# Kernel tuning notes

Hardware: AMD Instinct MI355X
Metric: run time of the kernel (lower is better)

## Reference

```python
import jax
jax.config.update("jax_enable_x64", True)
import jax.numpy as jnp
import numpy as np

CKA_WEIGHT = 0.1


def _group_cka_sum(feats):
    """feats: [F, N, D] float. Returns sum of pairwise CKA over all (i,j) pairs.

    Faithful to CKASR: K = X X^T with zeroed diagonal, unbiased HSIC
    (Song et al. estimator), CKA[i,j] = HSIC(Ki,Kj)/sqrt(HSIC(Ki,Ki)HSIC(Kj,Kj)).
    All pairwise loops are batched into einsums.
    """
    F, N, D = feats.shape
    X = feats.reshape(F, N, D).astype(jnp.float64)
    K = jnp.einsum('fnd,fmd->fnm', X, X)                 # [F,N,N] Gram
    K = K * (1.0 - jnp.eye(N, dtype=K.dtype))            # fill_diagonal_(0)
    # HSIC(Ki, Kj) = 1/(N(N-3)) * ( tr(Ki Kj)
    #   + sum(Ki) sum(Kj) / ((N-1)(N-2))
    #   - 2/(N-2) * <rowsum(Ki), rowsum(Kj)> )
    trKL = jnp.einsum('iab,jab->ij', K, K)               # tr(Ki Kj), K symmetric
    s = jnp.sum(K, axis=(1, 2))                          # [F] total sums
    r = jnp.sum(K, axis=2)                               # [F,N] row sums
    rr = jnp.einsum('ia,ja->ij', r, r)                   # [F,F]
    hsic = (trKL + jnp.outer(s, s) / ((N - 1) * (N - 2))
            - 2.0 * rr / (N - 2)) / (N * (N - 3))        # [F,F]
    d = jnp.sqrt(jnp.diagonal(hsic))                     # [F]
    cka = hsic / (d[:, None] * d[None, :])
    return jnp.sum(cka)


def setup_inputs() -> dict:
    key = jax.random.key(0)
    k1, k2, k3, k4 = jax.random.split(key, 4)
    N, C = 64, 1000
    output = jax.random.normal(k1, (N, C), dtype=jnp.float32)
    target = jax.random.randint(k2, (N,), 0, C, dtype=jnp.int64)
    feats_a = jax.random.normal(k3, (3, N, 65536), dtype=jnp.float32)
    feats_b = jax.random.normal(k4, (4, N, 32768), dtype=jnp.float32)
    return {"output": output, "target": target,
            "feats_a": feats_a, "feats_b": feats_b}


def reference(output, target, feats_a, feats_b):
    N = output.shape[0]
    logp = jax.nn.log_softmax(output.astype(jnp.float32), axis=-1)
    ce = -jnp.mean(logp[jnp.arange(N), target])           # CrossEntropyLoss (mean)
    cka = _group_cka_sum(feats_a) + _group_cka_sum(feats_b)
    loss = ce + CKA_WEIGHT * cka.astype(jnp.float32)
    return (loss, output)
```

## Files before the change

kernel.cpp:

```cpp
#include <hip/hip_runtime.h>
#include <math.h>

typedef __attribute__((ext_vector_type(8))) short short8;
typedef __attribute__((ext_vector_type(4))) float f32x4;
typedef __attribute__((ext_vector_type(16))) float f32x16;

#define PSTRIDE 4160

__device__ __forceinline__ unsigned int bf16_rn(float x) {
    unsigned int u = __float_as_uint(x);
    return (u + 0x7FFFu + ((u >> 16) & 1u)) >> 16;
}

__device__ __forceinline__ short8 cvt8(float4 a, float4 b) {
    short8 h;
    h[0] = (short)bf16_rn(a.x); h[1] = (short)bf16_rn(a.y);
    h[2] = (short)bf16_rn(a.z); h[3] = (short)bf16_rn(a.w);
    h[4] = (short)bf16_rn(b.x); h[5] = (short)bf16_rn(b.y);
    h[6] = (short)bf16_rn(b.z); h[7] = (short)bf16_rn(b.w);
    return h;
}

__global__ __launch_bounds__(512, 8) void gram_ce_kernel(
    const float* __restrict__ A, const float* __restrict__ B,
    float* __restrict__ partials, int nfA, int nfB,
    const float* __restrict__ logits, const int* __restrict__ target,
    float* __restrict__ out_copy, float* __restrict__ ce_rows, int ceCount)
{
    __shared__ float smem[4096];
    const int t = threadIdx.x;

    if ((int)blockIdx.x < ceCount) {
        const int row = blockIdx.x;
        const float* x = logits + row * 1000;
        float m = -INFINITY;
        for (int i = t; i < 1000; i += 512) {
            float v = x[i];
            out_copy[row * 1000 + i] = v;
            m = fmaxf(m, v);
        }
        smem[t] = m; __syncthreads();
        for (int s = 256; s > 0; s >>= 1) {
            if (t < s) smem[t] = fmaxf(smem[t], smem[t + s]);
            __syncthreads();
        }
        m = smem[0];
        __syncthreads();
        float ssum = 0.f;
        for (int i = t; i < 1000; i += 512) ssum += expf(x[i] - m);
        smem[t] = ssum; __syncthreads();
        for (int s = 256; s > 0; s >>= 1) {
            if (t < s) smem[t] += smem[t + s];
            __syncthreads();
        }
        if (t == 0) {
            double lse = (double)m + log((double)smem[0]);
            int tg = target[row];
            ce_rows[row] = (float)(-((double)x[tg] - lse));
        }
        return;
    }

    const int gb = blockIdx.x - ceCount;
    const int uA = nfA * 128;
    const float* xf;
    int c, D;
    if (gb < uA) {
        int f = gb >> 7; c = gb & 127; D = 65536;
        xf = A + (size_t)f * 64 * 65536;
    } else {
        int v = gb - uA;
        int f = v >> 6; c = v & 63; D = 32768;
        xf = B + (size_t)f * 64 * 32768;
    }

    const int wave = t >> 6, lane = t & 63;
    const int lr = lane & 31, hi = lane >> 5;

    f32x16 acc = (f32x16)0.f;
    if (wave < 4) {
        const int k0 = c * 512 + wave * 128 + hi * 8;
        const float* pA = xf + (size_t)lr * D + k0;
        const float* pB = xf + (size_t)(32 + lr) * D + k0;
#pragma unroll
        for (int s = 0; s < 8; ++s) {
            float4 a0 = *(const float4*)(pA + s * 16);
            float4 a1 = *(const float4*)(pA + s * 16 + 4);
            float4 b0 = *(const float4*)(pB + s * 16);
            float4 b1 = *(const float4*)(pB + s * 16 + 4);
            short8 fa = cvt8(a0, a1);
            short8 fb = cvt8(b0, b1);
            acc = __builtin_amdgcn_mfma_f32_32x32x16_bf16(fa, fb, acc, 0, 0, 0);
        }
    } else {
        const int rb = (wave >= 6) ? 32 : 0;
        const int k0 = c * 512 + (wave & 1) * 256 + hi * 8;
        const float* pA = xf + (size_t)(rb + lr) * D + k0;
#pragma unroll
        for (int s = 0; s < 16; ++s) {
            float4 a0 = *(const float4*)(pA + s * 16);
            float4 a1 = *(const float4*)(pA + s * 16 + 4);
            short8 fa = cvt8(a0, a1);
            acc = __builtin_amdgcn_mfma_f32_32x32x16_bf16(fa, fa, acc, 0, 0, 0);
        }
    }

    float* buf = (wave < 4) ? (smem + 2048)
               : ((wave < 6) ? smem : (smem + 1024));
    const bool writer = (wave == 0) || (wave == 4) || (wave == 6);
    if (writer) {
#pragma unroll
        for (int r = 0; r < 16; ++r) {
            int rl = (r & 3) + 8 * (r >> 2) + 4 * hi;
            buf[rl * 32 + lr] = acc[r];
        }
    }
    __syncthreads();
    if (!writer) {
#pragma unroll
        for (int r = 0; r < 16; ++r) {
            int rl = (r & 3) + 8 * (r >> 2) + 4 * hi;
            atomicAdd(&buf[rl * 32 + lr], acc[r]);
        }
    }
    __syncthreads();

    float* outp = partials + (size_t)gb * PSTRIDE;
    for (int e = t; e < 4096; e += 512) {
        int rr = e >> 6, cc = e & 63;
        float v;
        if (rr < 32)
            v = (cc < 32) ? smem[rr * 32 + cc]
                          : smem[2048 + rr * 32 + (cc - 32)];
        else
            v = (cc < 32) ? smem[2048 + cc * 32 + (rr - 32)]
                          : smem[1024 + (rr - 32) * 32 + (cc - 32)];
        outp[e] = v;
    }
}

__global__ __launch_bounds__(256) void reduce_kernel(
    const float* __restrict__ partials, float* __restrict__ K, int singleF)
{
    __shared__ double red[256];
    int f, eblk, base, count;
    if (singleF < 0) {
        f = blockIdx.x >> 6; eblk = blockIdx.x & 63;
        if (f < 3) { base = f * 128;            count = 128; }
        else       { base = 384 + (f - 3) * 64; count = 64;  }
    } else {
        f = singleF; eblk = blockIdx.x; base = 0;
        count = (f < 3) ? 128 : 64;
    }
    const int e = (eblk << 6) + (threadIdx.x & 63);
    const int jg = threadIdx.x >> 6;

    double s0 = 0.0, s1 = 0.0;
    for (int j = jg; j < count; j += 8) {
        s0 += (double)partials[(size_t)(base + j) * PSTRIDE + e];
        s1 += (double)partials[(size_t)(base + j + 4) * PSTRIDE + e];
    }
    red[threadIdx.x] = s0 + s1;
    __syncthreads();
    if (jg == 0) {
        double tot = red[threadIdx.x] + red[threadIdx.x + 64]
                   + red[threadIdx.x + 128] + red[threadIdx.x + 192];
        int rr = e >> 6, cc = e & 63;
        K[f * 4096 + e] = (rr == cc) ? 0.f : (float)tot;
    }
}

__global__ __launch_bounds__(256) void hsic_kernel(
    const float* __restrict__ K, double* __restrict__ hsic_out)
{
    const int p = blockIdx.x;
    int i, j;
    if (p < 9) { i = p / 3; j = p % 3; }
    else       { int q = p - 9; i = 3 + q / 4; j = 3 + q % 4; }
    const float* Ki = K + i * 4096;
    const float* Kj = K + j * 4096;
    const int t = threadIdx.x;

    __shared__ double red[256];
    __shared__ double ri[64], rj[64];

    double local = 0.0;
    for (int e = t; e < 4096; e += 256)
        local += (double)Ki[e] * (double)Kj[e];
    red[t] = local; __syncthreads();
    for (int s = 128; s > 0; s >>= 1) {
        if (t < s) red[t] += red[t + s];
        __syncthreads();
    }

    if (t < 64) {
        double s = 0.0;
        for (int mc = 0; mc < 64; ++mc) s += (double)Ki[t * 64 + mc];
        ri[t] = s;
    } else if (t < 128) {
        int n = t - 64;
        double s = 0.0;
        for (int mc = 0; mc < 64; ++mc) s += (double)Kj[n * 64 + mc];
        rj[n] = s;
    }
    __syncthreads();

    if (t == 0) {
        double tr = red[0];
        double rr = 0.0, si = 0.0, sj = 0.0;
        for (int n = 0; n < 64; ++n) {
            rr += ri[n] * rj[n];
            si += ri[n];
            sj += rj[n];
        }
        const double N = 64.0;
        const double c1 = (N - 1.0) * (N - 2.0);
        const double c2 = N - 2.0;
        const double c3 = N * (N - 3.0);
        hsic_out[p] = (tr + si * sj / c1 - 2.0 * rr / c2) / c3;
    }
}

__global__ __launch_bounds__(64) void final_kernel(
    const double* __restrict__ hsic, const float* __restrict__ ce_rows,
    float* __restrict__ out_loss)
{
    if (threadIdx.x != 0) return;
    double ce = 0.0;
    for (int n = 0; n < 64; ++n) ce += (double)ce_rows[n];
    ce /= 64.0;

    double cka_total = 0.0;
    for (int i = 0; i < 3; ++i)
        for (int j = 0; j < 3; ++j)
            cka_total += hsic[i * 3 + j] / sqrt(hsic[i * 3 + i] * hsic[j * 3 + j]);
    for (int i = 0; i < 4; ++i)
        for (int j = 0; j < 4; ++j)
            cka_total += hsic[9 + i * 4 + j] / sqrt(hsic[9 + i * 4 + i] * hsic[9 + j * 4 + j]);

    out_loss[0] = (float)(ce + 0.1 * cka_total);
}

extern "C" void kernel_launch(void* const* d_in, const int* in_sizes, int n_in,
                              void* d_out, int out_size, void* d_ws, size_t ws_size,
                              hipStream_t stream)
{
    const float* output  = (const float*)d_in[0];
    const int*   target  = (const int*)d_in[1];
    const float* feats_a = (const float*)d_in[2];
    const float* feats_b = (const float*)d_in[3];
    float* out = (float*)d_out;

    char* ws = (char*)d_ws;
    float*  K        = (float*)ws;
    float*  ce_rows  = (float*)(ws + 114688);
    double* hsic     = (double*)(ws + 114944);
    float*  partials = (float*)(ws + 131072);

    const size_t partMain = (size_t)640 * PSTRIDE * 4;
    const size_t mainNeed = 131072 + partMain;

    if (ws_size >= mainNeed) {
        hipLaunchKernelGGL(gram_ce_kernel, dim3(640 + 64), dim3(512), 0, stream,
                           feats_a, feats_b, partials, 3, 4,
                           output, target, out + 1, ce_rows, 64);
        hipLaunchKernelGGL(reduce_kernel, dim3(448), dim3(256), 0, stream,
                           partials, K, -1);
    } else {
        for (int f = 0; f < 7; ++f) {
            if (f < 3) {
                const float* X = feats_a + (size_t)f * 64 * 65536;
                int ce = (f == 0) ? 64 : 0;
                hipLaunchKernelGGL(gram_ce_kernel, dim3(128 + ce), dim3(512), 0, stream,
                                   X, (const float*)nullptr, partials, 1, 0,
                                   output, target, out + 1, ce_rows, ce);
            } else {
                const float* X = feats_b + (size_t)(f - 3) * 64 * 32768;
                hipLaunchKernelGGL(gram_ce_kernel, dim3(64), dim3(512), 0, stream,
                                   (const float*)nullptr, X, partials, 0, 1,
                                   output, target, out + 1, ce_rows, 0);
            }
            hipLaunchKernelGGL(reduce_kernel, dim3(64), dim3(256), 0, stream,
                               partials, K, f);
        }
    }

    hipLaunchKernelGGL(hsic_kernel, dim3(25), dim3(256), 0, stream, K, hsic);
    hipLaunchKernelGGL(final_kernel, dim3(1), dim3(64), 0, stream,
                       hsic, ce_rows, out);
}
```

Before: 160.3 us.

## Halve K-chunk per block, add register prefetch, pad shared-memory stride

Each block now covers 256 columns of the feature dimension instead of 512, which doubles the grid to 1280 Gram blocks and doubles the partial buffers the reduce kernel sums. The load loops now prefetch the next iteration's float4 values into registers so loads overlap the bf16 conversion and MFMA. The shared-memory tile stride is padded to 33 to avoid bank conflicts in the transposed readout, and the occupancy hint is lowered to 6. The intent is more parallelism and latency hiding for this memory-bound Gram computation, at the cost of twice as much partial write and reduce traffic.

Result: no change. 161.4 us (+0.7%).

```diff
diff --git a/kernel.cpp b/kernel.cpp
--- a/kernel.cpp
+++ b/kernel.cpp
@@ -6,6 +6,7 @@
 typedef __attribute__((ext_vector_type(16))) float f32x16;
 
 #define PSTRIDE 4160
+#define QSTRIDE 33
 
 __device__ __forceinline__ unsigned int bf16_rn(float x) {
     unsigned int u = __float_as_uint(x);
@@ -21,13 +22,13 @@
     return h;
 }
 
-__global__ __launch_bounds__(512, 8) void gram_ce_kernel(
+__global__ __launch_bounds__(512, 6) void gram_ce_kernel(
     const float* __restrict__ A, const float* __restrict__ B,
     float* __restrict__ partials, int nfA, int nfB,
     const float* __restrict__ logits, const int* __restrict__ target,
     float* __restrict__ out_copy, float* __restrict__ ce_rows, int ceCount)
 {
-    __shared__ float smem[4096];
+    __shared__ float smem[3328];
     const int t = threadIdx.x;
 
     if ((int)blockIdx.x < ceCount) {
@@ -62,15 +63,15 @@
     }
 
     const int gb = blockIdx.x - ceCount;
-    const int uA = nfA * 128;
+    const int uA = nfA * 256;
     const float* xf;
     int c, D;
     if (gb < uA) {
-        int f = gb >> 7; c = gb & 127; D = 65536;
+        int f = gb >> 8; c = gb & 255; D = 65536;
         xf = A + (size_t)f * 64 * 65536;
     } else {
         int v = gb - uA;
-        int f = v >> 6; c = v & 63; D = 32768;
+        int f = v >> 7; c = v & 127; D = 32768;
         xf = B + (size_t)f * 64 * 32768;
     }
 
@@ -79,40 +80,54 @@
 
     f32x16 acc = (f32x16)0.f;
     if (wave < 4) {
-        const int k0 = c * 512 + wave * 128 + hi * 8;
+        const int k0 = c * 256 + wave * 64 + hi * 8;
         const float* pA = xf + (size_t)lr * D + k0;
         const float* pB = xf + (size_t)(32 + lr) * D + k0;
+        float4 a0 = *(const float4*)(pA);
+        float4 a1 = *(const float4*)(pA + 4);
+        float4 b0 = *(const float4*)(pB);
+        float4 b1 = *(const float4*)(pB + 4);
 #pragma unroll
-        for (int s = 0; s < 8; ++s) {
-            float4 a0 = *(const float4*)(pA + s * 16);
-            float4 a1 = *(const float4*)(pA + s * 16 + 4);
-            float4 b0 = *(const float4*)(pB + s * 16);
-            float4 b1 = *(const float4*)(pB + s * 16 + 4);
+        for (int s = 0; s < 4; ++s) {
+            float4 na0, na1, nb0, nb1;
+            if (s < 3) {
+                na0 = *(const float4*)(pA + (s + 1) * 16);
+                na1 = *(const float4*)(pA + (s + 1) * 16 + 4);
+                nb0 = *(const float4*)(pB + (s + 1) * 16);
+                nb1 = *(const float4*)(pB + (s + 1) * 16 + 4);
+            }
             short8 fa = cvt8(a0, a1);
             short8 fb = cvt8(b0, b1);
             acc = __builtin_amdgcn_mfma_f32_32x32x16_bf16(fa, fb, acc, 0, 0, 0);
+            a0 = na0; a1 = na1; b0 = nb0; b1 = nb1;
         }
     } else {
         const int rb = (wave >= 6) ? 32 : 0;
-        const int k0 = c * 512 + (wave & 1) * 256 + hi * 8;
+        const int k0 = c * 256 + (wave & 1) * 128 + hi * 8;
         const float* pA = xf + (size_t)(rb + lr) * D + k0;
+        float4 a0 = *(const float4*)(pA);
+        float4 a1 = *(const float4*)(pA + 4);
 #pragma unroll
-        for (int s = 0; s < 16; ++s) {
-            float4 a0 = *(const float4*)(pA + s * 16);
-            float4 a1 = *(const float4*)(pA + s * 16 + 4);
+        for (int s = 0; s < 8; ++s) {
+            float4 na0, na1;
+            if (s < 7) {
+                na0 = *(const float4*)(pA + (s + 1) * 16);
+                na1 = *(const float4*)(pA + (s + 1) * 16 + 4);
+            }
             short8 fa = cvt8(a0, a1);
             acc = __builtin_amdgcn_mfma_f32_32x32x16_bf16(fa, fa, acc, 0, 0, 0);
-        }
-    }
-
-    float* buf = (wave < 4) ? (smem + 2048)
-               : ((wave < 6) ? smem : (smem + 1024));
+            a0 = na0; a1 = na1;
+        }
+    }
+
+    float* buf = (wave < 4) ? (smem + 2112)
+               : ((wave < 6) ? smem : (smem + 1056));
     const bool writer = (wave == 0) || (wave == 4) || (wave == 6);
     if (writer) {
 #pragma unroll
         for (int r = 0; r < 16; ++r) {
             int rl = (r & 3) + 8 * (r >> 2) + 4 * hi;
-            buf[rl * 32 + lr] = acc[r];
+            buf[rl * QSTRIDE + lr] = acc[r];
         }
     }
     __syncthreads();
@@ -120,7 +135,7 @@
 #pragma unroll
         for (int r = 0; r < 16; ++r) {
             int rl = (r & 3) + 8 * (r >> 2) + 4 * hi;
-            atomicAdd(&buf[rl * 32 + lr], acc[r]);
+            atomicAdd(&buf[rl * QSTRIDE + lr], acc[r]);
         }
     }
     __syncthreads();
@@ -130,11 +145,11 @@
         int rr = e >> 6, cc = e & 63;
         float v;
         if (rr < 32)
-            v = (cc < 32) ? smem[rr * 32 + cc]
-                          : smem[2048 + rr * 32 + (cc - 32)];
+            v = (cc < 32) ? smem[rr * QSTRIDE + cc]
+                          : smem[2112 + rr * QSTRIDE + (cc - 32)];
         else
-            v = (cc < 32) ? smem[2048 + cc * 32 + (rr - 32)]
-                          : smem[1024 + (rr - 32) * 32 + (cc - 32)];
+            v = (cc < 32) ? smem[2112 + cc * QSTRIDE + (rr - 32)]
+                          : smem[1056 + (rr - 32) * QSTRIDE + (cc - 32)];
         outp[e] = v;
     }
 }
@@ -146,11 +161,11 @@
     int f, eblk, base, count;
     if (singleF < 0) {
         f = blockIdx.x >> 6; eblk = blockIdx.x & 63;
-        if (f < 3) { base = f * 128;            count = 128; }
-        else       { base = 384 + (f - 3) * 64; count = 64;  }
+        if (f < 3) { base = f * 256;             count = 256; }
+        else       { base = 768 + (f - 3) * 128; count = 128; }
     } else {
         f = singleF; eblk = blockIdx.x; base = 0;
-        count = (f < 3) ? 128 : 64;
+        count = (f < 3) ? 256 : 128;
     }
     const int e = (eblk << 6) + (threadIdx.x & 63);
     const int jg = threadIdx.x >> 6;
@@ -257,11 +272,11 @@
     double* hsic     = (double*)(ws + 114944);
     float*  partials = (float*)(ws + 131072);
 
-    const size_t partMain = (size_t)640 * PSTRIDE * 4;
+    const size_t partMain = (size_t)1280 * PSTRIDE * 4;
     const size_t mainNeed = 131072 + partMain;
 
     if (ws_size >= mainNeed) {
-        hipLaunchKernelGGL(gram_ce_kernel, dim3(640 + 64), dim3(512), 0, stream,
+        hipLaunchKernelGGL(gram_ce_kernel, dim3(1280 + 64), dim3(512), 0, stream,
                            feats_a, feats_b, partials, 3, 4,
                            output, target, out + 1, ce_rows, 64);
         hipLaunchKernelGGL(reduce_kernel, dim3(448), dim3(256), 0, stream,
@@ -271,12 +286,12 @@
             if (f < 3) {
                 const float* X = feats_a + (size_t)f * 64 * 65536;
                 int ce = (f == 0) ? 64 : 0;
-                hipLaunchKernelGGL(gram_ce_kernel, dim3(128 + ce), dim3(512), 0, stream,
+                hipLaunchKernelGGL(gram_ce_kernel, dim3(256 + ce), dim3(512), 0, stream,
                                    X, (const float*)nullptr, partials, 1, 0,
                                    output, target, out + 1, ce_rows, ce);
             } else {
                 const float* X = feats_b + (size_t)(f - 3) * 64 * 32768;
-                hipLaunchKernelGGL(gram_ce_kernel, dim3(64), dim3(512), 0, stream,
+                hipLaunchKernelGGL(gram_ce_kernel, dim3(128), dim3(512), 0, stream,
                                    (const float*)nullptr, X, partials, 0, 1,
                                    output, target, out + 1, ce_rows, 0);
             }
```

## Give every wave all three Gram sub-blocks over its own K slice

Applied to the files above, without the earlier changes.

Before, the 512-thread block split work unevenly across waves: four waves computed the off-diagonal 32x32 tile over 128-wide K slices and four computed the diagonal tiles over 256-wide slices. Now every wave loads both row halves for its own 64-wide K slice and issues three MFMAs (off-diagonal plus both diagonal tiles), so each element is loaded once per block and all waves carry equal work. The LDS reduction now spans three padded buffers (stride 33, to avoid bank conflicts), with seven waves atomically adding into each. This triples accumulator registers per wave and adds shared-memory atomics, and the occupancy hint in launch bounds is lowered to compensate.

Result: slower. 207.4 us (+29.4%).

```diff
diff --git a/kernel.cpp b/kernel.cpp
--- a/kernel.cpp
+++ b/kernel.cpp
@@ -6,6 +6,7 @@
 typedef __attribute__((ext_vector_type(16))) float f32x16;
 
 #define PSTRIDE 4160
+#define QSTRIDE 33
 
 __device__ __forceinline__ unsigned int bf16_rn(float x) {
     unsigned int u = __float_as_uint(x);
@@ -21,13 +22,13 @@
     return h;
 }
 
-__global__ __launch_bounds__(512, 8) void gram_ce_kernel(
+__global__ __launch_bounds__(512, 4) void gram_ce_kernel(
     const float* __restrict__ A, const float* __restrict__ B,
     float* __restrict__ partials, int nfA, int nfB,
     const float* __restrict__ logits, const int* __restrict__ target,
     float* __restrict__ out_copy, float* __restrict__ ce_rows, int ceCount)
 {
-    __shared__ float smem[4096];
+    __shared__ float smem[3328];
     const int t = threadIdx.x;
 
     if ((int)blockIdx.x < ceCount) {
@@ -76,51 +77,45 @@
 
     const int wave = t >> 6, lane = t & 63;
     const int lr = lane & 31, hi = lane >> 5;
-
-    f32x16 acc = (f32x16)0.f;
-    if (wave < 4) {
-        const int k0 = c * 512 + wave * 128 + hi * 8;
-        const float* pA = xf + (size_t)lr * D + k0;
-        const float* pB = xf + (size_t)(32 + lr) * D + k0;
+    const int k0 = c * 512 + wave * 64 + hi * 8;
+
+    const float* pA = xf + (size_t)lr * D + k0;
+    const float* pB = xf + (size_t)(32 + lr) * D + k0;
+
+    f32x16 aOD = (f32x16)0.f;
+    f32x16 aD0 = (f32x16)0.f;
+    f32x16 aD1 = (f32x16)0.f;
+
 #pragma unroll
-        for (int s = 0; s < 8; ++s) {
-            float4 a0 = *(const float4*)(pA + s * 16);
-            float4 a1 = *(const float4*)(pA + s * 16 + 4);
-            float4 b0 = *(const float4*)(pB + s * 16);
-            float4 b1 = *(const float4*)(pB + s * 16 + 4);
-            short8 fa = cvt8(a0, a1);
-            short8 fb = cvt8(b0, b1);
-            acc = __builtin_amdgcn_mfma_f32_32x32x16_bf16(fa, fb, acc, 0, 0, 0);
-        }
-    } else {
-        const int rb = (wave >= 6) ? 32 : 0;
-        const int k0 = c * 512 + (wave & 1) * 256 + hi * 8;
-        const float* pA = xf + (size_t)(rb + lr) * D + k0;
-#pragma unroll
-        for (int s = 0; s < 16; ++s) {
-            float4 a0 = *(const float4*)(pA + s * 16);
-            float4 a1 = *(const float4*)(pA + s * 16 + 4);
-            short8 fa = cvt8(a0, a1);
-            acc = __builtin_amdgcn_mfma_f32_32x32x16_bf16(fa, fa, acc, 0, 0, 0);
-        }
-    }
-
-    float* buf = (wave < 4) ? (smem + 2048)
-               : ((wave < 6) ? smem : (smem + 1024));
-    const bool writer = (wave == 0) || (wave == 4) || (wave == 6);
-    if (writer) {
+    for (int s = 0; s < 4; ++s) {
+        float4 a0 = *(const float4*)(pA + s * 16);
+        float4 a1 = *(const float4*)(pA + s * 16 + 4);
+        float4 b0 = *(const float4*)(pB + s * 16);
+        float4 b1 = *(const float4*)(pB + s * 16 + 4);
+        short8 fa = cvt8(a0, a1);
+        short8 fb = cvt8(b0, b1);
+        aOD = __builtin_amdgcn_mfma_f32_32x32x16_bf16(fa, fb, aOD, 0, 0, 0);
+        aD0 = __builtin_amdgcn_mfma_f32_32x32x16_bf16(fa, fa, aD0, 0, 0, 0);
+        aD1 = __builtin_amdgcn_mfma_f32_32x32x16_bf16(fb, fb, aD1, 0, 0, 0);
+    }
+
+    if (wave == 0) {
 #pragma unroll
         for (int r = 0; r < 16; ++r) {
-            int rl = (r & 3) + 8 * (r >> 2) + 4 * hi;
-            buf[rl * 32 + lr] = acc[r];
-        }
-    }
-    __syncthreads();
-    if (!writer) {
+            int rl = ((r & 3) + 8 * (r >> 2) + 4 * hi) * QSTRIDE + lr;
+            smem[rl] = aD0[r];
+            smem[1056 + rl] = aD1[r];
+            smem[2112 + rl] = aOD[r];
+        }
+    }
+    __syncthreads();
+    if (wave != 0) {
 #pragma unroll
         for (int r = 0; r < 16; ++r) {
-            int rl = (r & 3) + 8 * (r >> 2) + 4 * hi;
-            atomicAdd(&buf[rl * 32 + lr], acc[r]);
+            int rl = ((r & 3) + 8 * (r >> 2) + 4 * hi) * QSTRIDE + lr;
+            atomicAdd(&smem[rl], aD0[r]);
+            atomicAdd(&smem[1056 + rl], aD1[r]);
+            atomicAdd(&smem[2112 + rl], aOD[r]);
         }
     }
     __syncthreads();
@@ -130,11 +125,11 @@
         int rr = e >> 6, cc = e & 63;
         float v;
         if (rr < 32)
-            v = (cc < 32) ? smem[rr * 32 + cc]
-                          : smem[2048 + rr * 32 + (cc - 32)];
+            v = (cc < 32) ? smem[rr * QSTRIDE + cc]
+                          : smem[2112 + rr * QSTRIDE + (cc - 32)];
         else
-            v = (cc < 32) ? smem[2048 + cc * 32 + (rr - 32)]
-                          : smem[1024 + (rr - 32) * 32 + (cc - 32)];
+            v = (cc < 32) ? smem[2112 + cc * QSTRIDE + (rr - 32)]
+                          : smem[1056 + (rr - 32) * QSTRIDE + (cc - 32)];
         outp[e] = v;
     }
 }
```
